# Kernel optimization log

Hardware: AMD Instinct MI355X
Metric: run time of the kernel (lower is better)

The kernel has to match this reference:

```python
import jax, jax.numpy as jnp
import numpy as np

B_BOXES = 5
N_CLASSES = 80
LAMBDA_COORD = 5.0
LAMBDA_NOOBJ = 0.5
LAMBDA_CLASS = 1.0
EPS = 1e-6


def _corners(b):
    # b: (..., 4) center-format (x, y, w, h) -> x1, y1, x2, y2
    x, y, w, h = b[..., 0], b[..., 1], b[..., 2], b[..., 3]
    return x - w / 2, y - h / 2, x + w / 2, y + h / 2


def pairwise_iou(p_box, t_box):
    # p_box, t_box: (N, S, S, B, 4) -> ious: (N, S, S, B_pred, B_tgt)
    px1, py1, px2, py2 = _corners(p_box[..., :, None, :])
    tx1, ty1, tx2, ty2 = _corners(t_box[..., None, :, :])
    iw = jnp.clip(jnp.minimum(px2, tx2) - jnp.maximum(px1, tx1), 0.0)
    ih = jnp.clip(jnp.minimum(py2, ty2) - jnp.maximum(py1, ty1), 0.0)
    inter = iw * ih
    area_p = (px2 - px1) * (py2 - py1)
    area_t = (tx2 - tx1) * (ty2 - ty1)
    return inter / (area_p + area_t - inter + EPS)


def setup_inputs() -> dict:
    key = jax.random.key(0)
    k1, k2 = jax.random.split(key)
    N, S = 128, 26
    ch = B_BOXES * (5 + N_CLASSES)  # 425
    preds = jax.random.normal(k1, (N, S, S, ch), dtype=jnp.float32)
    targets = jax.random.normal(k2, (N, S, S, ch), dtype=jnp.float32)
    return {"preds": preds, "targets": targets}


def reference(preds, targets):
    N, S = preds.shape[0], preds.shape[1]
    D = 5 + N_CLASSES
    p = preds.reshape(N, S, S, B_BOXES, D)
    t = targets.reshape(N, S, S, B_BOXES, D)

    ious = pairwise_iou(p[..., :4], t[..., :4])          # (N,S,S,B,B)
    best = jnp.argmax(ious, axis=-1)                      # (N,S,S,B)
    idx = jnp.broadcast_to(best[..., None], t.shape)
    matched = jnp.take_along_axis(t, idx, axis=3)         # (N,S,S,B,D)

    obj = (matched[..., 4] > 0).astype(p.dtype)           # (N,S,S,B)
    noobj = 1.0 - obj

    xy_loss = LAMBDA_COORD * jnp.sum(obj[..., None] * (p[..., 0:2] - matched[..., 0:2]) ** 2)

    pwh = jnp.sqrt(jnp.abs(p[..., 2:4] + EPS))
    twh = jnp.sqrt(jnp.abs(matched[..., 2:4] + EPS))
    wh_loss = LAMBDA_COORD * jnp.sum(obj[..., None] * (pwh - twh) ** 2)

    conf_sq = (p[..., 4] - matched[..., 4]) ** 2
    conf_loss_obj = jnp.sum(obj * conf_sq)
    conf_loss_noobj = LAMBDA_NOOBJ * jnp.sum(noobj * conf_sq)

    tcls = jnp.argmax(t[..., 5:], axis=-1)                # (N,S,S,B)
    logp = jax.nn.log_softmax(p[..., 5:], axis=-1)
    nll = -jnp.take_along_axis(logp, tcls[..., None], axis=-1)[..., 0]
    class_loss = LAMBDA_CLASS * jnp.sum(obj * nll)

    return xy_loss + wh_loss + conf_loss_obj + conf_loss_noobj + class_loss
```

## Files before the change

kernel.cpp:

```cpp
#include <hip/hip_runtime.h>
#include <math.h>

#define NB 5
#define NC 80
#define DD 85
#define CH 425
#define EPSF 1e-6f
#define TPB 256
#define GRID 2048

__global__ __launch_bounds__(TPB) void yolo_loss_kernel(
    const float* __restrict__ preds,
    const float* __restrict__ targets,
    float* __restrict__ partials,
    int nboxes,
    int use_atomic)
{
    const int tid     = threadIdx.x;
    const int q       = tid & 3;
    const int quad0   = (blockIdx.x * TPB + tid) >> 2;
    const int qstride = (gridDim.x * TPB) >> 2;

    float acc = 0.0f;

    for (int g = quad0; g < nboxes; g += qstride) {
        const int base = g * DD;
        const int kb   = base + 5 + q * 20;

        float s  = 0.0f;
        float bv = -INFINITY;
        int   bi = 0x7fffffff;
        float bp = 0.0f;
        #pragma unroll
        for (int k = 0; k < 20; ++k) {
            const float pl = preds[kb + k];
            const float tl = targets[kb + k];
            s += __expf(pl);
            if (tl > bv) { bv = tl; bi = q * 20 + k; bp = pl; }
        }
        #pragma unroll
        for (int m = 1; m < 4; m <<= 1) {
            s += __shfl_xor(s, m, 64);
            const float ov = __shfl_xor(bv, m, 64);
            const int   oi = __shfl_xor(bi, m, 64);
            const float op = __shfl_xor(bp, m, 64);
            if (ov > bv || (ov == bv && oi < bi)) { bv = ov; bi = oi; bp = op; }
        }

        if (q == 0) {
            const float nll = __logf(s) - bp;

            const int cell = g / 5;
            const float px = preds[base + 0], py = preds[base + 1],
                        pw = preds[base + 2], ph = preds[base + 3],
                        pconf = preds[base + 4];
            const float px1 = px - pw * 0.5f, py1 = py - ph * 0.5f;
            const float px2 = px + pw * 0.5f, py2 = py + ph * 0.5f;
            const float area_p = (px2 - px1) * (py2 - py1);

            float best = -INFINITY;
            float mx = 0.f, my = 0.f, mw = 0.f, mh = 0.f, mconf = 0.f;
            #pragma unroll
            for (int j = 0; j < NB; ++j) {
                const int tb = (cell * NB + j) * DD;
                const float tx = targets[tb + 0], ty = targets[tb + 1],
                            tw = targets[tb + 2], th = targets[tb + 3],
                            tcf = targets[tb + 4];
                const float tx1 = tx - tw * 0.5f, ty1 = ty - th * 0.5f;
                const float tx2 = tx + tw * 0.5f, ty2 = ty + th * 0.5f;
                float iw = fminf(px2, tx2) - fmaxf(px1, tx1); iw = fmaxf(iw, 0.0f);
                float ih = fminf(py2, ty2) - fmaxf(py1, ty1); ih = fmaxf(ih, 0.0f);
                const float inter  = iw * ih;
                const float area_t = (tx2 - tx1) * (ty2 - ty1);
                const float iou    = inter / (area_p + area_t - inter + EPSF);
                if (iou > best) { best = iou; mx = tx; my = ty; mw = tw; mh = th; mconf = tcf; }
            }

            const float obj = (mconf > 0.0f) ? 1.0f : 0.0f;
            const float dx = px - mx, dy = py - my;
            float term = 5.0f * obj * (dx * dx + dy * dy);
            const float dw = sqrtf(fabsf(pw + EPSF)) - sqrtf(fabsf(mw + EPSF));
            const float dh = sqrtf(fabsf(ph + EPSF)) - sqrtf(fabsf(mh + EPSF));
            term += 5.0f * obj * (dw * dw + dh * dh);
            const float dc  = pconf - mconf;
            const float csq = dc * dc;
            term += obj * csq + 0.5f * (1.0f - obj) * csq;
            term += obj * nll;
            acc += term;
        }
    }

    __shared__ float s_wsum[4];
    #pragma unroll
    for (int off = 32; off > 0; off >>= 1) acc += __shfl_down(acc, off, 64);
    if ((tid & 63) == 0) s_wsum[tid >> 6] = acc;
    __syncthreads();
    if (tid == 0) {
        const float v = s_wsum[0] + s_wsum[1] + s_wsum[2] + s_wsum[3];
        if (use_atomic) atomicAdd(partials, v);
        else            partials[blockIdx.x] = v;
    }
}

__global__ __launch_bounds__(TPB) void reduce_kernel(
    const float* __restrict__ partials, float* __restrict__ out, int n)
{
    float s = 0.0f;
    for (int i = threadIdx.x; i < n; i += TPB) s += partials[i];
    #pragma unroll
    for (int off = 32; off > 0; off >>= 1) s += __shfl_down(s, off, 64);
    __shared__ float wsum[4];
    if ((threadIdx.x & 63) == 0) wsum[threadIdx.x >> 6] = s;
    __syncthreads();
    if (threadIdx.x == 0) out[0] = wsum[0] + wsum[1] + wsum[2] + wsum[3];
}

extern "C" void kernel_launch(void* const* d_in, const int* in_sizes, int n_in,
                              void* d_out, int out_size, void* d_ws, size_t ws_size,
                              hipStream_t stream) {
    const float* preds   = (const float*)d_in[0];
    const float* targets = (const float*)d_in[1];
    float* out = (float*)d_out;

    const int ncells = in_sizes[0] / CH;
    const int nboxes = ncells * NB;
    const int blocks = GRID;

    if (ws_size >= (size_t)blocks * sizeof(float)) {
        float* ws = (float*)d_ws;
        yolo_loss_kernel<<<blocks, TPB, 0, stream>>>(preds, targets, ws, nboxes, 0);
        reduce_kernel<<<1, TPB, 0, stream>>>(ws, out, blocks);
    } else {
        hipMemsetAsync(out, 0, sizeof(float), stream);
        yolo_loss_kernel<<<blocks, TPB, 0, stream>>>(preds, targets, out, nboxes, 1);
    }
}
```

Measured before the change: 313.0 us.

## Stage two-cell chunks per wave through LDS with register prefetch of next chunk

Each wave now loads a two-cell chunk of preds and targets with coalesced float2 loads into registers, writes it to LDS, and prefetches the next chunk while computing from LDS. This replaces the strided per-quad global loads, which were poorly coalesced and reread target box headers. The cost is added LDS traffic and register pressure. Only 40 of 64 lanes do work in the compute phase, and the chunk split assumes an even cell count.

```diff
diff --git a/kernel.cpp b/kernel.cpp
--- a/kernel.cpp
+++ b/kernel.cpp
@@ -7,93 +7,142 @@
 #define CH 425
 #define EPSF 1e-6f
 #define TPB 256
-#define GRID 2048
+#define WPB 4
+#define CPC 2
+#define CHUNK_F (CPC * CH)
+#define CHUNK_F2 (CHUNK_F / 2)
+#define LROUNDS 7
+#define TASKS (CPC * NB)
+#define MAXBLK 1280
 
 __global__ __launch_bounds__(TPB) void yolo_loss_kernel(
     const float* __restrict__ preds,
     const float* __restrict__ targets,
     float* __restrict__ partials,
-    int nboxes,
+    int nchunks,
     int use_atomic)
 {
-    const int tid     = threadIdx.x;
-    const int q       = tid & 3;
-    const int quad0   = (blockIdx.x * TPB + tid) >> 2;
-    const int qstride = (gridDim.x * TPB) >> 2;
+    __shared__ __align__(16) float s_p[WPB][CHUNK_F];
+    __shared__ __align__(16) float s_t[WPB][CHUNK_F];
+    __shared__ float s_wsum[WPB];
+
+    const int tid  = threadIdx.x;
+    const int wave = tid >> 6;
+    const int lane = tid & 63;
+
+    float* lp = s_p[wave];
+    float* lt = s_t[wave];
+
+    const int wid     = blockIdx.x * WPB + wave;
+    const int wstride = gridDim.x * WPB;
+
+    const float2* gp2 = (const float2*)preds;
+    const float2* gt2 = (const float2*)targets;
+
+    float2 rp[LROUNDS], rt[LROUNDS];
 
     float acc = 0.0f;
+    int c = wid;
 
-    for (int g = quad0; g < nboxes; g += qstride) {
-        const int base = g * DD;
-        const int kb   = base + 5 + q * 20;
-
-        float s  = 0.0f;
-        float bv = -INFINITY;
-        int   bi = 0x7fffffff;
-        float bp = 0.0f;
+    if (c < nchunks) {
+        const int gb = c * CHUNK_F2;
         #pragma unroll
-        for (int k = 0; k < 20; ++k) {
-            const float pl = preds[kb + k];
-            const float tl = targets[kb + k];
-            s += __expf(pl);
-            if (tl > bv) { bv = tl; bi = q * 20 + k; bp = pl; }
-        }
-        #pragma unroll
-        for (int m = 1; m < 4; m <<= 1) {
-            s += __shfl_xor(s, m, 64);
-            const float ov = __shfl_xor(bv, m, 64);
-            const int   oi = __shfl_xor(bi, m, 64);
-            const float op = __shfl_xor(bp, m, 64);
-            if (ov > bv || (ov == bv && oi < bi)) { bv = ov; bi = oi; bp = op; }
-        }
-
-        if (q == 0) {
-            const float nll = __logf(s) - bp;
-
-            const int cell = g / 5;
-            const float px = preds[base + 0], py = preds[base + 1],
-                        pw = preds[base + 2], ph = preds[base + 3],
-                        pconf = preds[base + 4];
-            const float px1 = px - pw * 0.5f, py1 = py - ph * 0.5f;
-            const float px2 = px + pw * 0.5f, py2 = py + ph * 0.5f;
-            const float area_p = (px2 - px1) * (py2 - py1);
-
-            float best = -INFINITY;
-            float mx = 0.f, my = 0.f, mw = 0.f, mh = 0.f, mconf = 0.f;
-            #pragma unroll
-            for (int j = 0; j < NB; ++j) {
-                const int tb = (cell * NB + j) * DD;
-                const float tx = targets[tb + 0], ty = targets[tb + 1],
-                            tw = targets[tb + 2], th = targets[tb + 3],
-                            tcf = targets[tb + 4];
-                const float tx1 = tx - tw * 0.5f, ty1 = ty - th * 0.5f;
-                const float tx2 = tx + tw * 0.5f, ty2 = ty + th * 0.5f;
-                float iw = fminf(px2, tx2) - fmaxf(px1, tx1); iw = fmaxf(iw, 0.0f);
-                float ih = fminf(py2, ty2) - fmaxf(py1, ty1); ih = fmaxf(ih, 0.0f);
-                const float inter  = iw * ih;
-                const float area_t = (tx2 - tx1) * (ty2 - ty1);
-                const float iou    = inter / (area_p + area_t - inter + EPSF);
-                if (iou > best) { best = iou; mx = tx; my = ty; mw = tw; mh = th; mconf = tcf; }
-            }
-
-            const float obj = (mconf > 0.0f) ? 1.0f : 0.0f;
-            const float dx = px - mx, dy = py - my;
-            float term = 5.0f * obj * (dx * dx + dy * dy);
-            const float dw = sqrtf(fabsf(pw + EPSF)) - sqrtf(fabsf(mw + EPSF));
-            const float dh = sqrtf(fabsf(ph + EPSF)) - sqrtf(fabsf(mh + EPSF));
-            term += 5.0f * obj * (dw * dw + dh * dh);
-            const float dc  = pconf - mconf;
-            const float csq = dc * dc;
-            term += obj * csq + 0.5f * (1.0f - obj) * csq;
-            term += obj * nll;
-            acc += term;
+        for (int r = 0; r < LROUNDS; ++r) {
+            const int idx = r * 64 + lane;
+            if (idx < CHUNK_F2) { rp[r] = gp2[gb + idx]; rt[r] = gt2[gb + idx]; }
         }
     }
 
-    __shared__ float s_wsum[4];
+    for (; c < nchunks; c += wstride) {
+        #pragma unroll
+        for (int r = 0; r < LROUNDS; ++r) {
+            const int idx = r * 64 + lane;
+            if (idx < CHUNK_F2) {
+                ((float2*)lp)[idx] = rp[r];
+                ((float2*)lt)[idx] = rt[r];
+            }
+        }
+        const int cn = c + wstride;
+        if (cn < nchunks) {
+            const int gb = cn * CHUNK_F2;
+            #pragma unroll
+            for (int r = 0; r < LROUNDS; ++r) {
+                const int idx = r * 64 + lane;
+                if (idx < CHUNK_F2) { rp[r] = gp2[gb + idx]; rt[r] = gt2[gb + idx]; }
+            }
+        }
+
+        const int t = lane >> 2;
+        const int q = lane & 3;
+        if (t < TASKS) {
+            const int pb = t * DD;
+            const int kb = pb + 5 + q * 20;
+
+            float s  = 0.0f;
+            float bv = -INFINITY;
+            int   bi = 0x7fffffff;
+            float bp = 0.0f;
+            #pragma unroll 5
+            for (int k = 0; k < 20; ++k) {
+                const float pl = lp[kb + k];
+                const float tl = lt[kb + k];
+                s += __expf(pl);
+                if (tl > bv) { bv = tl; bi = q * 20 + k; bp = pl; }
+            }
+            #pragma unroll
+            for (int m = 1; m < 4; m <<= 1) {
+                s += __shfl_xor(s, m, 64);
+                const float ov = __shfl_xor(bv, m, 64);
+                const int   oi = __shfl_xor(bi, m, 64);
+                const float op = __shfl_xor(bp, m, 64);
+                if (ov > bv || (ov == bv && oi < bi)) { bv = ov; bi = oi; bp = op; }
+            }
+
+            if (q == 0) {
+                const float nll = __logf(s) - bp;
+
+                const int cellbase = (t / NB) * CH;
+                const float px = lp[pb + 0], py = lp[pb + 1], pw = lp[pb + 2],
+                            ph = lp[pb + 3], pconf = lp[pb + 4];
+                const float px1 = px - pw * 0.5f, py1 = py - ph * 0.5f;
+                const float px2 = px + pw * 0.5f, py2 = py + ph * 0.5f;
+                const float area_p = (px2 - px1) * (py2 - py1);
+
+                float best = -INFINITY;
+                float mx = 0.f, my = 0.f, mw = 0.f, mh = 0.f, mconf = 0.f;
+                #pragma unroll
+                for (int j = 0; j < NB; ++j) {
+                    const int tb = cellbase + j * DD;
+                    const float tx = lt[tb + 0], ty = lt[tb + 1], tw = lt[tb + 2],
+                                th = lt[tb + 3], tcf = lt[tb + 4];
+                    const float tx1 = tx - tw * 0.5f, ty1 = ty - th * 0.5f;
+                    const float tx2 = tx + tw * 0.5f, ty2 = ty + th * 0.5f;
+                    float iw = fminf(px2, tx2) - fmaxf(px1, tx1); iw = fmaxf(iw, 0.0f);
+                    float ih = fminf(py2, ty2) - fmaxf(py1, ty1); ih = fmaxf(ih, 0.0f);
+                    const float inter  = iw * ih;
+                    const float area_t = (tx2 - tx1) * (ty2 - ty1);
+                    const float iou    = inter / (area_p + area_t - inter + EPSF);
+                    if (iou > best) { best = iou; mx = tx; my = ty; mw = tw; mh = th; mconf = tcf; }
+                }
+
+                const float obj = (mconf > 0.0f) ? 1.0f : 0.0f;
+                const float dx = px - mx, dy = py - my;
+                float term = 5.0f * obj * (dx * dx + dy * dy);
+                const float dw = sqrtf(fabsf(pw + EPSF)) - sqrtf(fabsf(mw + EPSF));
+                const float dh = sqrtf(fabsf(ph + EPSF)) - sqrtf(fabsf(mh + EPSF));
+                term += 5.0f * obj * (dw * dw + dh * dh);
+                const float dc  = pconf - mconf;
+                const float csq = dc * dc;
+                term += obj * csq + 0.5f * (1.0f - obj) * csq;
+                term += obj * nll;
+                acc += term;
+            }
+        }
+    }
+
     #pragma unroll
     for (int off = 32; off > 0; off >>= 1) acc += __shfl_down(acc, off, 64);
-    if ((tid & 63) == 0) s_wsum[tid >> 6] = acc;
+    if (lane == 0) s_wsum[wave] = acc;
     __syncthreads();
     if (tid == 0) {
         const float v = s_wsum[0] + s_wsum[1] + s_wsum[2] + s_wsum[3];
@@ -122,16 +171,16 @@
     const float* targets = (const float*)d_in[1];
     float* out = (float*)d_out;
 
-    const int ncells = in_sizes[0] / CH;
-    const int nboxes = ncells * NB;
-    const int blocks = GRID;
+    const int ncells  = in_sizes[0] / CH;
+    const int nchunks = ncells / CPC;
+    const int blocks  = MAXBLK;
 
     if (ws_size >= (size_t)blocks * sizeof(float)) {
         float* ws = (float*)d_ws;
-        yolo_loss_kernel<<<blocks, TPB, 0, stream>>>(preds, targets, ws, nboxes, 0);
+        yolo_loss_kernel<<<blocks, TPB, 0, stream>>>(preds, targets, ws, nchunks, 0);
         reduce_kernel<<<1, TPB, 0, stream>>>(ws, out, blocks);
     } else {
         hipMemsetAsync(out, 0, sizeof(float), stream);
-        yolo_loss_kernel<<<blocks, TPB, 0, stream>>>(preds, targets, out, nboxes, 1);
+        yolo_loss_kernel<<<blocks, TPB, 0, stream>>>(preds, targets, out, nchunks, 1);
     }
 }
```

Measured after the change: 309.1 us. About the same (-1.3%).

## Load class logits as aligned float4 vectors using per-phase box alignment

Applied to the files above, without the earlier changes.

Splits the box loop into four phases by box index mod 4. Each phase has a fixed 4-float alignment offset for its class logits, so each of the four threads can fetch its 20 logits through aligned float4 loads, read through compile-time component selection, instead of scalar loads. The grid size also drops from 2048 to 1536 blocks. In exchange it issues a few extra vector loads per box, uses more registers, and assumes the box count is divisible by 4, since any remainder boxes are skipped.

```diff
diff --git a/kernel.cpp b/kernel.cpp
--- a/kernel.cpp
+++ b/kernel.cpp
@@ -7,40 +7,54 @@
 #define CH 425
 #define EPSF 1e-6f
 #define TPB 256
-#define GRID 2048
+#define GRID 1536
 
-__global__ __launch_bounds__(TPB) void yolo_loss_kernel(
-    const float* __restrict__ preds,
-    const float* __restrict__ targets,
-    float* __restrict__ partials,
-    int nboxes,
-    int use_atomic)
+#define CSEL(v, c) ((c) == 0 ? (v).x : (c) == 1 ? (v).y : (c) == 2 ? (v).z : (v).w)
+
+#define CLS_STEP(j) {                                              \
+    const float pl = CSEL(pv[(S + (j)) >> 2], (S + (j)) & 3);      \
+    const float tl = CSEL(tv[(S + (j)) >> 2], (S + (j)) & 3);      \
+    se += __expf(pl);                                              \
+    if (tl > bv) { bv = tl; bi = q * 20 + (j); bp = pl; } }
+
+template<int R>
+__device__ __forceinline__ float phase_acc(const float* __restrict__ preds,
+                                           const float* __restrict__ targets,
+                                           int nboxes, int quad0, int qstride,
+                                           int q)
 {
-    const int tid     = threadIdx.x;
-    const int q       = tid & 3;
-    const int quad0   = (blockIdx.x * TPB + tid) >> 2;
-    const int qstride = (gridDim.x * TPB) >> 2;
+    constexpr int S   = (R + 1) & 3;
+    constexpr int NF4 = (S == 0) ? 5 : 6;
+    const int nphase = nboxes >> 2;
+
+    const float4* p4 = (const float4*)preds;
+    const float4* t4 = (const float4*)targets;
 
     float acc = 0.0f;
 
-    for (int g = quad0; g < nboxes; g += qstride) {
-        const int base = g * DD;
-        const int kb   = base + 5 + q * 20;
+    for (int t = quad0; t < nphase; t += qstride) {
+        const int g = R + 4 * t;
+        const size_t F = (((size_t)g * DD + 5 - S) >> 2) + (size_t)(5 * q);
 
-        float s  = 0.0f;
+        float4 pv[6], tv[6];
+        #pragma unroll
+        for (int k = 0; k < NF4; ++k) {
+            pv[k] = p4[F + k];
+            tv[k] = t4[F + k];
+        }
+
+        float se = 0.0f;
         float bv = -INFINITY;
         int   bi = 0x7fffffff;
         float bp = 0.0f;
-        #pragma unroll
-        for (int k = 0; k < 20; ++k) {
-            const float pl = preds[kb + k];
-            const float tl = targets[kb + k];
-            s += __expf(pl);
-            if (tl > bv) { bv = tl; bi = q * 20 + k; bp = pl; }
-        }
+        CLS_STEP(0)  CLS_STEP(1)  CLS_STEP(2)  CLS_STEP(3)  CLS_STEP(4)
+        CLS_STEP(5)  CLS_STEP(6)  CLS_STEP(7)  CLS_STEP(8)  CLS_STEP(9)
+        CLS_STEP(10) CLS_STEP(11) CLS_STEP(12) CLS_STEP(13) CLS_STEP(14)
+        CLS_STEP(15) CLS_STEP(16) CLS_STEP(17) CLS_STEP(18) CLS_STEP(19)
+
         #pragma unroll
         for (int m = 1; m < 4; m <<= 1) {
-            s += __shfl_xor(s, m, 64);
+            se += __shfl_xor(se, m, 64);
             const float ov = __shfl_xor(bv, m, 64);
             const int   oi = __shfl_xor(bi, m, 64);
             const float op = __shfl_xor(bp, m, 64);
@@ -48,9 +62,9 @@
         }
 
         if (q == 0) {
-            const float nll = __logf(s) - bp;
+            const float nll = __logf(se) - bp;
 
-            const int cell = g / 5;
+            const size_t base = (size_t)g * DD;
             const float px = preds[base + 0], py = preds[base + 1],
                         pw = preds[base + 2], ph = preds[base + 3],
                         pconf = preds[base + 4];
@@ -58,11 +72,12 @@
             const float px2 = px + pw * 0.5f, py2 = py + ph * 0.5f;
             const float area_p = (px2 - px1) * (py2 - py1);
 
+            const int cell = g / 5;
             float best = -INFINITY;
             float mx = 0.f, my = 0.f, mw = 0.f, mh = 0.f, mconf = 0.f;
             #pragma unroll
             for (int j = 0; j < NB; ++j) {
-                const int tb = (cell * NB + j) * DD;
+                const size_t tb = ((size_t)cell * NB + j) * DD;
                 const float tx = targets[tb + 0], ty = targets[tb + 1],
                             tw = targets[tb + 2], th = targets[tb + 3],
                             tcf = targets[tb + 4];
@@ -89,6 +104,26 @@
             acc += term;
         }
     }
+    return acc;
+}
+
+__global__ __launch_bounds__(TPB) void yolo_loss_kernel(
+    const float* __restrict__ preds,
+    const float* __restrict__ targets,
+    float* __restrict__ partials,
+    int nboxes,
+    int use_atomic)
+{
+    const int tid     = threadIdx.x;
+    const int q       = tid & 3;
+    const int quad0   = (blockIdx.x * TPB + tid) >> 2;
+    const int qstride = (gridDim.x * TPB) >> 2;
+
+    float acc = 0.0f;
+    acc += phase_acc<0>(preds, targets, nboxes, quad0, qstride, q);
+    acc += phase_acc<1>(preds, targets, nboxes, quad0, qstride, q);
+    acc += phase_acc<2>(preds, targets, nboxes, quad0, qstride, q);
+    acc += phase_acc<3>(preds, targets, nboxes, quad0, qstride, q);
 
     __shared__ float s_wsum[4];
     #pragma unroll
```

Result: slower. 336.3 us (+7.4%).
